# Performance work log

Measured on AMD Instinct MI355X. Metric: run time of the kernel, lower is better.

Reference implementation:

```python
import jax, jax.numpy as jnp
import numpy as np

H = 2048        # hidden_nodes
T = 8192        # timeseries length
WASHOUT = 200
SPECTRAL_RADIUS = 0.9


def setup_inputs() -> dict:
    key = jax.random.key(0)
    k1, k2, k3 = jax.random.split(key, 3)
    u = jax.random.normal(k1, (T,), dtype=jnp.float32)
    # w_res ~ uniform(-0.5, 0.5), rescaled to approximate spectral radius 0.9
    w_res = jax.random.uniform(k2, (H, H), dtype=jnp.float32) - 0.5
    unif_std = 1.0 / np.sqrt(12.0)
    w_res = w_res * np.float32(SPECTRAL_RADIUS / (unif_std * np.sqrt(H)))
    # w_in ~ uniform(-0.5, 0.5) * input_scaling(=1.0)
    w_in = jax.random.uniform(k3, (H,), dtype=jnp.float32) - 0.5
    w_out = jnp.ones((H,), dtype=jnp.float32)
    # w_out_density = 1.0 -> mask covers all nodes (identity gather)
    w_out_mask = jnp.arange(H, dtype=jnp.int32)
    return {"u": u, "w_res": w_res, "w_in": w_in, "w_out": w_out,
            "w_out_mask": w_out_mask, "washout": WASHOUT}


def reference(u, w_res, w_in, w_out, w_out_mask, washout):
    # Inference path (y=None, awgn_test_std=0, adc_quantization=None):
    #   x_{t} = tanh(w_in * u_t + w_res @ x_{t-1}); X[t] = x_t[mask]
    #   return X[washout:] @ w_out
    def step(x, u_t):
        x = jnp.tanh(w_in * u_t + w_res @ x)   # [H]
        return x, x[w_out_mask]                # carry, per-step readout row

    x0 = jnp.zeros((w_res.shape[0],), dtype=u.dtype)
    _, X = jax.lax.scan(step, x0, u)           # X: [T, output_dim]
    return X[washout:] @ w_out                 # [T - washout]
```

## Files before the change

kernel.cpp:

```cpp
#include <hip/hip_runtime.h>
#include <math.h>


#define H_   2048
#define RPB  8
#define NBLK 256

__global__ void esn_zero(float* __restrict__ p, int n)
{
    int i = blockIdx.x * blockDim.x + threadIdx.x;
    int stride = gridDim.x * blockDim.x;
    for (; i < n; i += stride) p[i] = 0.0f;
}

__global__ __launch_bounds__(1024) void esn_scatter_c(const int* __restrict__ mask,
                                                      const float* __restrict__ w_out,
                                                      float* __restrict__ ws_f, int H)
{
    float* c = ws_f + 2 * H_;
    for (int i = threadIdx.x; i < H; i += blockDim.x)
        atomicAdd(&c[mask[i]], w_out[i]);
}

__global__ __launch_bounds__(256) void esn_run(const float* __restrict__ u,
                                               const float* __restrict__ w_res,
                                               const float* __restrict__ w_in,
                                               float* __restrict__ out,
                                               float* __restrict__ ws_f,
                                               int T, int washout, int use_part)
{
    __shared__ float Wlds[RPB * H_];
    __shared__ float xs[H_];
    __shared__ float psum[4];

    const int tid  = threadIdx.x;
    const int wave = tid >> 6;
    const int lane = tid & 63;
    const int bid  = blockIdx.x;
    const int r0 = 2 * wave, r1 = 2 * wave + 1;
    const int grow0 = bid * RPB + r0, grow1 = bid * RPB + r1;

    {
        const float4* src = (const float4*)(w_res + (size_t)bid * RPB * H_);
        float4* dst = (float4*)Wlds;
        for (int i = tid; i < RPB * H_ / 4; i += 256) dst[i] = src[i];
    }
    float win0 = 0.f, win1 = 0.f, c0 = 0.f, c1 = 0.f;
    if (lane == 0) {
        win0 = w_in[grow0]; win1 = w_in[grow1];
        c0 = ws_f[2 * H_ + grow0]; c1 = ws_f[2 * H_ + grow1];
    }

    float* buf0 = ws_f;
    float* buf1 = ws_f + H_;
    unsigned* arr    = (unsigned*)(ws_f + 8192);
    unsigned* flags  = (unsigned*)(ws_f + 16384);
    unsigned* myarr  = arr   + bid * 32;
    unsigned* myflag = flags + bid * 32;
    float* part = ws_f + 24576;
    const int detector = (bid == 0);

    const float4* w0p = (const float4*)(Wlds + r0 * H_);
    const float4* w1p = (const float4*)(Wlds + r1 * H_);
    const float4* xs4 = (const float4*)xs;

    int broken = 0;
    float u_next = u[0];
    __syncthreads();

    for (int k = 0; k < T; ++k) {
        const float* xsrc = (k & 1) ? buf1 : buf0;
        float*       xdst = (k & 1) ? buf0 : buf1;
#pragma unroll
        for (int i = 0; i < 8; ++i) {
            int j = (i << 8) + tid;
            xs[j] = __hip_atomic_load(xsrc + j, __ATOMIC_RELAXED,
                                      __HIP_MEMORY_SCOPE_AGENT);
        }
        float uk = u_next;
        if (k + 1 < T) u_next = u[k + 1];
        __syncthreads();

        float4 a0 = {0.f,0.f,0.f,0.f}, a1 = {0.f,0.f,0.f,0.f};
#pragma unroll
        for (int c = 0; c < 8; ++c) {
            float4 xv  = xs4[c * 64 + lane];
            float4 wv0 = w0p[c * 64 + lane];
            float4 wv1 = w1p[c * 64 + lane];
            a0.x = fmaf(wv0.x, xv.x, a0.x); a0.y = fmaf(wv0.y, xv.y, a0.y);
            a0.z = fmaf(wv0.z, xv.z, a0.z); a0.w = fmaf(wv0.w, xv.w, a0.w);
            a1.x = fmaf(wv1.x, xv.x, a1.x); a1.y = fmaf(wv1.y, xv.y, a1.y);
            a1.z = fmaf(wv1.z, xv.z, a1.z); a1.w = fmaf(wv1.w, xv.w, a1.w);
        }
        float s0 = (a0.x + a0.y) + (a0.z + a0.w);
        float s1 = (a1.x + a1.y) + (a1.z + a1.w);
#pragma unroll
        for (int d = 1; d < 64; d <<= 1) {
            s0 += __shfl_xor(s0, d);
            s1 += __shfl_xor(s1, d);
        }

        if (lane == 0) {
            float z0 = fmaf(win0, uk, s0);
            float z1 = fmaf(win1, uk, s1);
            z0 = fminf(fmaxf(z0, -15.f), 15.f);
            z1 = fminf(fmaxf(z1, -15.f), 15.f);
            float e0 = __expf(2.f * z0), e1 = __expf(2.f * z1);
            float t0 = (e0 - 1.f) / (e0 + 1.f), t1 = (e1 - 1.f) / (e1 + 1.f);
            __hip_atomic_store(xdst + grow0, t0, __ATOMIC_RELAXED,
                               __HIP_MEMORY_SCOPE_AGENT);
            __hip_atomic_store(xdst + grow1, t1, __ATOMIC_RELAXED,
                               __HIP_MEMORY_SCOPE_AGENT);
            psum[wave] = c0 * t0 + c1 * t1;
        }
        asm volatile("s_waitcnt vmcnt(0)" ::: "memory");
        __syncthreads();

        if (wave == 0) {
            if (lane == 0)
                __hip_atomic_store(myarr, (unsigned)(k + 1), __ATOMIC_RELAXED,
                                   __HIP_MEMORY_SCOPE_AGENT);
            if (lane == 0) {
                float pw = (psum[0] + psum[1]) + (psum[2] + psum[3]);
                if (use_part) part[(size_t)k * NBLK + bid] = pw;
                else if (k >= washout) atomicAdd(&out[k - washout], pw);
            }

            if (detector) {
                unsigned target = (unsigned)(k + 1);
                if (!broken) {
                    int spins = 0;
                    for (;;) {
                        unsigned v0 = __hip_atomic_load(arr + (lane)       * 32, __ATOMIC_RELAXED, __HIP_MEMORY_SCOPE_AGENT);
                        unsigned v1 = __hip_atomic_load(arr + (lane +  64) * 32, __ATOMIC_RELAXED, __HIP_MEMORY_SCOPE_AGENT);
                        unsigned v2 = __hip_atomic_load(arr + (lane + 128) * 32, __ATOMIC_RELAXED, __HIP_MEMORY_SCOPE_AGENT);
                        unsigned v3 = __hip_atomic_load(arr + (lane + 192) * 32, __ATOMIC_RELAXED, __HIP_MEMORY_SCOPE_AGENT);
                        if (__all(v0 >= target && v1 >= target &&
                                  v2 >= target && v3 >= target)) break;
                        if (++spins > 1000000) { broken = 1; break; }
                    }
                }
#pragma unroll
                for (int i = 0; i < 4; ++i)
                    __hip_atomic_store(flags + (lane + i * 64) * 32, target,
                                       __ATOMIC_RELAXED, __HIP_MEMORY_SCOPE_AGENT);
            } else if (!broken) {
                unsigned target = (unsigned)(k + 1);
                int spins = 0;
                for (;;) {
                    unsigned v = __hip_atomic_load(myflag, __ATOMIC_RELAXED,
                                                   __HIP_MEMORY_SCOPE_AGENT);
                    if (v >= target) break;
                    if (++spins > 4000000) { broken = 1; break; }
                    __builtin_amdgcn_s_sleep(1);
                }
            }
        }
        __syncthreads();
    }
}

__global__ __launch_bounds__(256) void esn_reduce(const float* __restrict__ part,
                                                  float* __restrict__ out,
                                                  int out_size, int washout)
{
    int wv = threadIdx.x >> 6, lane = threadIdx.x & 63;
    int t = blockIdx.x * 4 + wv;
    if (t >= out_size) return;
    const float4* p = (const float4*)(part + (size_t)(t + washout) * NBLK);
    float4 v = p[lane];
    float s = (v.x + v.y) + (v.z + v.w);
#pragma unroll
    for (int d = 1; d < 64; d <<= 1) s += __shfl_xor(s, d);
    if (lane == 0) out[t] = s;
}

extern "C" void kernel_launch(void* const* d_in, const int* in_sizes, int n_in,
                              void* d_out, int out_size, void* d_ws, size_t ws_size,
                              hipStream_t stream)
{
    const float* u     = (const float*)d_in[0];
    const float* w_res = (const float*)d_in[1];
    const float* w_in  = (const float*)d_in[2];
    const float* w_out = (const float*)d_in[3];
    const int*   mask  = (const int*)d_in[4];
    int T = in_sizes[0];
    int H = in_sizes[2];
    int washout = T - out_size;
    float* out  = (float*)d_out;
    float* ws_f = (float*)d_ws;

    size_t need = (size_t)(24576 + (size_t)T * NBLK) * 4;
    int use_part = (ws_size >= need) ? 1 : 0;

    hipLaunchKernelGGL(esn_zero, dim3(64), dim3(256), 0, stream, ws_f, 24576);
    if (!use_part)
        hipLaunchKernelGGL(esn_zero, dim3(32), dim3(256), 0, stream, out, out_size);
    hipLaunchKernelGGL(esn_scatter_c, dim3(1), dim3(1024), 0, stream, mask, w_out, ws_f, H);

    void* args[] = { (void*)&u, (void*)&w_res, (void*)&w_in, (void*)&out,
                     (void*)&ws_f, (void*)&T, (void*)&washout, (void*)&use_part };
    hipError_t e = hipLaunchCooperativeKernel((const void*)esn_run,
                                              dim3(NBLK), dim3(256),
                                              args, 0, stream);
    if (e != hipSuccess) {
        hipLaunchKernelGGL(esn_run, dim3(NBLK), dim3(256), 0, stream,
                           u, w_res, w_in, out, ws_f, T, washout, use_part);
    }
    if (use_part)
        hipLaunchKernelGGL(esn_reduce, dim3((out_size + 3) / 4), dim3(256), 0, stream,
                           ws_f + 24576, out, out_size, washout);
}
```

Measured before the change: 40.91 ms.

## Replace centralized grid barrier with per-element step-tagged values

Each state element is now stored as a 64-bit word holding the step index in its upper half and the float value in its lower half, and it is double-buffered. Consumers spin on each element until its tag matches the current step. This removes the detector-block barrier, the flag broadcast, and the extra block syncs and vmcnt wait that every step paid. In exchange, global state traffic doubles and every thread polls, which adds L2 contention. Relaxed ordering makes correctness depend on the packed 64-bit store being atomic.

```diff
diff --git a/kernel.cpp b/kernel.cpp
--- a/kernel.cpp
+++ b/kernel.cpp
@@ -5,6 +5,7 @@
 #define H_   2048
 #define RPB  8
 #define NBLK 256
+typedef unsigned long long ull;
 
 __global__ void esn_zero(float* __restrict__ p, int n)
 {
@@ -17,7 +18,7 @@
                                                       const float* __restrict__ w_out,
                                                       float* __restrict__ ws_f, int H)
 {
-    float* c = ws_f + 2 * H_;
+    float* c = ws_f + 8192;
     for (int i = threadIdx.x; i < H; i += blockDim.x)
         atomicAdd(&c[mask[i]], w_out[i]);
 }
@@ -48,37 +49,40 @@
     float win0 = 0.f, win1 = 0.f, c0 = 0.f, c1 = 0.f;
     if (lane == 0) {
         win0 = w_in[grow0]; win1 = w_in[grow1];
-        c0 = ws_f[2 * H_ + grow0]; c1 = ws_f[2 * H_ + grow1];
+        c0 = ws_f[8192 + grow0]; c1 = ws_f[8192 + grow1];
     }
 
-    float* buf0 = ws_f;
-    float* buf1 = ws_f + H_;
-    unsigned* arr    = (unsigned*)(ws_f + 8192);
-    unsigned* flags  = (unsigned*)(ws_f + 16384);
-    unsigned* myarr  = arr   + bid * 32;
-    unsigned* myflag = flags + bid * 32;
-    float* part = ws_f + 24576;
-    const int detector = (bid == 0);
+    ull* pairs = (ull*)ws_f;
+    float* part = ws_f + 10240;
 
     const float4* w0p = (const float4*)(Wlds + r0 * H_);
     const float4* w1p = (const float4*)(Wlds + r1 * H_);
     const float4* xs4 = (const float4*)xs;
 
-    int broken = 0;
     float u_next = u[0];
     __syncthreads();
 
     for (int k = 0; k < T; ++k) {
-        const float* xsrc = (k & 1) ? buf1 : buf0;
-        float*       xdst = (k & 1) ? buf0 : buf1;
+        const ull* sp = pairs + (k & 1) * H_;
+        ull*       dp = pairs + ((k + 1) & 1) * H_;
+        float uk = u_next;
+        if (k + 1 < T) u_next = u[k + 1];
+
+        ull pv[8];
+#pragma unroll
+        for (int i = 0; i < 8; ++i)
+            pv[i] = __hip_atomic_load(sp + (i << 8) + tid, __ATOMIC_RELAXED,
+                                      __HIP_MEMORY_SCOPE_AGENT);
 #pragma unroll
         for (int i = 0; i < 8; ++i) {
-            int j = (i << 8) + tid;
-            xs[j] = __hip_atomic_load(xsrc + j, __ATOMIC_RELAXED,
-                                      __HIP_MEMORY_SCOPE_AGENT);
+            int spins = 0;
+            while ((unsigned)(pv[i] >> 32) != (unsigned)k) {
+                pv[i] = __hip_atomic_load(sp + (i << 8) + tid, __ATOMIC_RELAXED,
+                                          __HIP_MEMORY_SCOPE_AGENT);
+                if (++spins > 2000000) break;
+            }
+            xs[(i << 8) + tid] = __uint_as_float((unsigned)pv[i]);
         }
-        float uk = u_next;
-        if (k + 1 < T) u_next = u[k + 1];
         __syncthreads();
 
         float4 a0 = {0.f,0.f,0.f,0.f}, a1 = {0.f,0.f,0.f,0.f};
@@ -107,56 +111,21 @@
             z1 = fminf(fmaxf(z1, -15.f), 15.f);
             float e0 = __expf(2.f * z0), e1 = __expf(2.f * z1);
             float t0 = (e0 - 1.f) / (e0 + 1.f), t1 = (e1 - 1.f) / (e1 + 1.f);
-            __hip_atomic_store(xdst + grow0, t0, __ATOMIC_RELAXED,
+            ull p0 = ((ull)(unsigned)(k + 1) << 32) | (ull)__float_as_uint(t0);
+            ull p1 = ((ull)(unsigned)(k + 1) << 32) | (ull)__float_as_uint(t1);
+            __hip_atomic_store(dp + grow0, p0, __ATOMIC_RELAXED,
                                __HIP_MEMORY_SCOPE_AGENT);
-            __hip_atomic_store(xdst + grow1, t1, __ATOMIC_RELAXED,
+            __hip_atomic_store(dp + grow1, p1, __ATOMIC_RELAXED,
                                __HIP_MEMORY_SCOPE_AGENT);
             psum[wave] = c0 * t0 + c1 * t1;
         }
-        asm volatile("s_waitcnt vmcnt(0)" ::: "memory");
         __syncthreads();
 
-        if (wave == 0) {
-            if (lane == 0)
-                __hip_atomic_store(myarr, (unsigned)(k + 1), __ATOMIC_RELAXED,
-                                   __HIP_MEMORY_SCOPE_AGENT);
-            if (lane == 0) {
-                float pw = (psum[0] + psum[1]) + (psum[2] + psum[3]);
-                if (use_part) part[(size_t)k * NBLK + bid] = pw;
-                else if (k >= washout) atomicAdd(&out[k - washout], pw);
-            }
-
-            if (detector) {
-                unsigned target = (unsigned)(k + 1);
-                if (!broken) {
-                    int spins = 0;
-                    for (;;) {
-                        unsigned v0 = __hip_atomic_load(arr + (lane)       * 32, __ATOMIC_RELAXED, __HIP_MEMORY_SCOPE_AGENT);
-                        unsigned v1 = __hip_atomic_load(arr + (lane +  64) * 32, __ATOMIC_RELAXED, __HIP_MEMORY_SCOPE_AGENT);
-                        unsigned v2 = __hip_atomic_load(arr + (lane + 128) * 32, __ATOMIC_RELAXED, __HIP_MEMORY_SCOPE_AGENT);
-                        unsigned v3 = __hip_atomic_load(arr + (lane + 192) * 32, __ATOMIC_RELAXED, __HIP_MEMORY_SCOPE_AGENT);
-                        if (__all(v0 >= target && v1 >= target &&
-                                  v2 >= target && v3 >= target)) break;
-                        if (++spins > 1000000) { broken = 1; break; }
-                    }
-                }
-#pragma unroll
-                for (int i = 0; i < 4; ++i)
-                    __hip_atomic_store(flags + (lane + i * 64) * 32, target,
-                                       __ATOMIC_RELAXED, __HIP_MEMORY_SCOPE_AGENT);
-            } else if (!broken) {
-                unsigned target = (unsigned)(k + 1);
-                int spins = 0;
-                for (;;) {
-                    unsigned v = __hip_atomic_load(myflag, __ATOMIC_RELAXED,
-                                                   __HIP_MEMORY_SCOPE_AGENT);
-                    if (v >= target) break;
-                    if (++spins > 4000000) { broken = 1; break; }
-                    __builtin_amdgcn_s_sleep(1);
-                }
-            }
+        if (tid == 0) {
+            float pw = (psum[0] + psum[1]) + (psum[2] + psum[3]);
+            if (use_part) part[(size_t)k * NBLK + bid] = pw;
+            else if (k >= washout) atomicAdd(&out[k - washout], pw);
         }
-        __syncthreads();
     }
 }
 
@@ -190,10 +159,10 @@
     float* out  = (float*)d_out;
     float* ws_f = (float*)d_ws;
 
-    size_t need = (size_t)(24576 + (size_t)T * NBLK) * 4;
+    size_t need = (size_t)(10240 + (size_t)T * NBLK) * 4;
     int use_part = (ws_size >= need) ? 1 : 0;
 
-    hipLaunchKernelGGL(esn_zero, dim3(64), dim3(256), 0, stream, ws_f, 24576);
+    hipLaunchKernelGGL(esn_zero, dim3(64), dim3(256), 0, stream, ws_f, 10240);
     if (!use_part)
         hipLaunchKernelGGL(esn_zero, dim3(32), dim3(256), 0, stream, out, out_size);
     hipLaunchKernelGGL(esn_scatter_c, dim3(1), dim3(1024), 0, stream, mask, w_out, ws_f, H);
@@ -209,5 +178,5 @@
     }
     if (use_part)
         hipLaunchKernelGGL(esn_reduce, dim3((out_size + 3) / 4), dim3(256), 0, stream,
-                           ws_f + 24576, out, out_size, washout);
+                           ws_f + 10240, out, out_size, washout);
 }
```

Result: no change. 40.73 ms (-0.4%).
